# Kernel tuning notes

Measured on AMD Instinct MI355X. Metric: run time of the kernel, lower is better.

Reference implementation:

```python
import jax, jax.numpy as jnp
import numpy as np

N, C, T = 64, 512, 64
P = N * (N - 1) // 2  # 2016 pairs


def _maxpool2x2(h):
    p, c, H, W = h.shape
    return h.reshape(p, c, H // 2, 2, W // 2, 2).max(axis=(3, 5))


def setup_inputs() -> dict:
    key = jax.random.key(0)
    ks = jax.random.split(key, 16)
    s = lambda k, shape, fan: jax.random.normal(k, shape, jnp.float32) * (1.0 / np.sqrt(fan))
    return {
        "x": jax.random.normal(ks[0], (N, C, T), jnp.float32),
        "w_conv1d": s(ks[1], (256, 512), 512),  # Conv1d(512,256,k=1) weight squeezed
        "b_conv1d": jnp.zeros((256,), jnp.float32),
        "w_c1": s(ks[2], (32, 512), 512),       # Conv2d(512,32,1x1)
        "b_c1": jnp.zeros((32,), jnp.float32),
        "w_c2": s(ks[3], (8, 32), 32),          # Conv2d(32,8,1x1)
        "b_c2": jnp.zeros((8,), jnp.float32),
        "w_fc1": s(ks[4], (32, 64), 64),
        "b_fc1": jnp.zeros((32,), jnp.float32),
        "w_fc2": s(ks[5], (8, 32), 32),
        "b_fc2": jnp.zeros((8,), jnp.float32),
        "w_fc3": s(ks[6], (1, 8), 8),
        "b_fc3": jnp.zeros((1,), jnp.float32),
        "w_mlp": s(ks[7], (1, C * T), C * T),   # stand-in my_fc: Linear(512*T,1)
        "b_mlp": jnp.zeros((1,), jnp.float32),
    }


def reference(x, w_conv1d, b_conv1d, w_c1, b_c1, w_c2, b_c2,
              w_fc1, b_fc1, w_fc2, b_fc2, w_fc3, b_fc3, w_mlp, b_mlp):
    # per-sample score head (my_fc stand-in)
    score = jax.nn.sigmoid(x.reshape(N, -1) @ w_mlp.T + b_mlp)  # [N,1]
    # shared conv1d over all samples at once (original does it per-pair)
    f = jnp.einsum("nct,oc->not", x, w_conv1d) + b_conv1d[None, :, None]  # [N,256,T]
    ii, jj = jnp.triu_indices(N, k=1)  # P pairs, same order as the nested loop
    # pairwise correlation matrix: einsum('abd,acd->abc')
    M = jnp.einsum("pct,pdt->pcd", f[ii], f[jj])  # [P,256,256]
    M = M.reshape(P, 512, 32, 4)
    h = jnp.einsum("pchw,oc->pohw", M, w_c1) + b_c1[None, :, None, None]
    h = _maxpool2x2(h)  # [P,32,16,2]
    h = jnp.einsum("pchw,oc->pohw", h, w_c2) + b_c2[None, :, None, None]
    h = _maxpool2x2(h)  # [P,8,8,1]
    v = h.reshape(P, 64)
    v = jax.nn.relu(v @ w_fc1.T + b_fc1)
    v = jax.nn.relu(v @ w_fc2.T + b_fc2)
    group_score = jax.nn.sigmoid(v @ w_fc3.T + b_fc3).reshape(-1)  # [P]
    return score, group_score
```

## Files before the change

### kernel.cpp

```cpp
#include <hip/hip_runtime.h>
#include <hip/hip_bf16.h>
#include <math.h>


typedef __attribute__((ext_vector_type(8))) short short8;
typedef __attribute__((ext_vector_type(4))) float f32x4;

__device__ __forceinline__ unsigned short f2bf(float f) {
    __hip_bfloat16 h = __float2bfloat16(f);
    return *reinterpret_cast<unsigned short*>(&h);
}

__global__ __launch_bounds__(256) void k_prep(
    const float* __restrict__ x, const float* __restrict__ w_conv1d,
    const float* __restrict__ b_conv1d, const float* __restrict__ w_c1,
    const float* __restrict__ w_mlp,
    unsigned short* __restrict__ xxTf, unsigned short* __restrict__ Wbf,
    float* __restrict__ Gb, float* __restrict__ part)
{
    __shared__ float sf[64 * 65];
    int u = blockIdx.x, tid = threadIdx.x;

    if (u < 128) {
        int idx = u * 256 + tid;
        int m = idx >> 7, c4 = (idx & 127) * 4;
        float4 v = *reinterpret_cast<const float4*>(w_conv1d + m * 512 + c4);
        ushort4 uu;
        uu.x = f2bf(v.x); uu.y = f2bf(v.y); uu.z = f2bf(v.z); uu.w = f2bf(v.w);
        int mt = m >> 4, r15 = m & 15;
        int kc = c4 >> 5, k8 = (c4 >> 3) & 3, rem = c4 & 7;
        *reinterpret_cast<ushort4*>(
            Wbf + ((mt * 16 + kc) * 64 + k8 * 16 + r15) * 8 + rem) = uu;
    } else if (u < 256) {
        int b = u - 128;
        int r = b >> 1;
        int cin = (b & 1) * 256 + tid;
        int s = r >> 5, o = r & 31;
        const float* wrow = w_c1 + o * 512 + s;
        const float* wcp  = w_conv1d + cin;
        float pq[4];
        #pragma unroll
        for (int q = 0; q < 4; ++q) {
            float acc = 0.f;
            #pragma unroll 8
            for (int c = q * 64; c < q * 64 + 64; ++c)
                acc += wrow[2 * c] * wcp[c * 512];
            pq[q] = acc;
        }
        float v = ((pq[0] + pq[1]) + pq[2]) + pq[3];
        int m = 256 + r;
        int mt = m >> 4, r15 = m & 15;
        int kc = cin >> 5, k8 = (cin >> 3) & 3, rem = cin & 7;
        Wbf[((mt * 16 + kc) * 64 + k8 * 16 + r15) * 8 + rem] = f2bf(v);
    } else if (u == 256) {
        float* abred = sf;
        Gb[tid] = b_conv1d[tid];
        int r = tid & 63, q = tid >> 6;
        int s = r >> 5, o = r & 31;
        const float* wr2 = w_c1 + o * 512 + s;
        float a = 0.f;
        #pragma unroll 8
        for (int c = q * 64; c < q * 64 + 64; ++c)
            a += wr2[2 * c] * b_conv1d[c];
        abred[tid] = a;
        __syncthreads();
        if (tid < 64)
            Gb[256 + tid] = abred[tid] + abred[tid + 64]
                          + abred[tid + 128] + abred[tid + 192];
    } else if (u < 769) {
        int v = u - 257;
        int n = v >> 3, c0 = (v & 7) * 64;
        float* tile = sf;
        int cl = tid >> 4, t4 = (tid & 15) * 4;
        const float* xp = x + n * 32768 + c0 * 64;
        #pragma unroll
        for (int pp = 0; pp < 4; ++pp) {
            int c = cl + pp * 16;
            float4 vv = *reinterpret_cast<const float4*>(xp + c * 64 + t4);
            tile[(t4 + 0) * 65 + c] = vv.x; tile[(t4 + 1) * 65 + c] = vv.y;
            tile[(t4 + 2) * 65 + c] = vv.z; tile[(t4 + 3) * 65 + c] = vv.w;
        }
        __syncthreads();
        int tl = tid >> 4, cl4 = (tid & 15) * 4;
        int c = c0 + cl4;
        int kc = c >> 5, k8 = (c >> 3) & 3, rem = c & 7;
        #pragma unroll
        for (int pp = 0; pp < 4; ++pp) {
            int t = tl + pp * 16;
            ushort4 uu;
            uu.x = f2bf(tile[t * 65 + cl4 + 0]);
            uu.y = f2bf(tile[t * 65 + cl4 + 1]);
            uu.z = f2bf(tile[t * 65 + cl4 + 2]);
            uu.w = f2bf(tile[t * 65 + cl4 + 3]);
            *reinterpret_cast<ushort4*>(
                xxTf + n * 32768 + ((pp * 16 + kc) * 64 + k8 * 16 + tl) * 8 + rem) = uu;
        }
    } else {
        int v = u - 769;
        int n = v >> 2, c4 = v & 3;
        const float4* x4 = reinterpret_cast<const float4*>(x + n * 32768) + c4 * 2048;
        const float4* w4 = reinterpret_cast<const float4*>(w_mlp) + c4 * 2048;
        float acc = 0.f;
        for (int uu = tid; uu < 2048; uu += 256) {
            float4 a = x4[uu], w = w4[uu];
            acc += a.x * w.x + a.y * w.y + a.z * w.z + a.w * w.w;
        }
        for (int off = 32; off; off >>= 1) acc += __shfl_down(acc, off, 64);
        float* red = sf;
        if ((tid & 63) == 0) red[tid >> 6] = acc;
        __syncthreads();
        if (tid == 0)
            part[n * 4 + c4] = red[0] + red[1] + red[2] + red[3];
    }
}

__global__ __launch_bounds__(256) void k_fgemm(
    const unsigned short* __restrict__ Wbf, const unsigned short* __restrict__ xxTf,
    const float* __restrict__ Gb, unsigned short* __restrict__ FTTb,
    unsigned short* __restrict__ ALb)
{
    int n = blockIdx.x, mg = blockIdx.y, nt = blockIdx.z;
    int tid = threadIdx.x, l = tid & 63, w = tid >> 6;
    int mt = mg * 4 + w;
    int m0 = mt * 16;
    int t0 = nt * 16;
    int r15 = l & 15, kg = l >> 4;
    const unsigned short* ap = Wbf + (size_t)mt * 16 * 512 + l * 8;
    const unsigned short* bp = xxTf + (size_t)n * 32768 + (size_t)nt * 16 * 512 + l * 8;
    f32x4 acc = {0.f, 0.f, 0.f, 0.f};
    #pragma unroll
    for (int ks = 0; ks < 16; ++ks) {
        short8 a = *reinterpret_cast<const short8*>(ap + ks * 512);
        short8 b = *reinterpret_cast<const short8*>(bp + ks * 512);
        acc = __builtin_amdgcn_mfma_f32_16x16x32_bf16(a, b, acc, 0, 0, 0);
    }
    int t = t0 + r15;
    int mrow = m0 + kg * 4;
    float4 gb = *reinterpret_cast<const float4*>(Gb + mrow);
    float gbv[4] = {gb.x, gb.y, gb.z, gb.w};
    if (m0 < 256) {
        #pragma unroll
        for (int r = 0; r < 4; ++r) {
            int m = mrow + r;
            int e = m & 127, s = m >> 7, kp = s * 64 + t;
            int off = (((e << 8) + (kp << 1)) ^ ((e & 7) << 4)) >> 1;
            FTTb[n * 16384 + off] = f2bf(acc[r] + gbv[r]);
        }
    } else {
        #pragma unroll
        for (int r = 0; r < 4; ++r) {
            int m = mrow + r;
            int rr = m - 256, o = rr & 31, sA = rr >> 5, kp = sA * 64 + t;
            int off = (((o << 8) + (kp << 1)) ^ ((o & 7) << 4)) >> 1;
            ALb[n * 4096 + off] = f2bf(acc[r] + gbv[r]);
        }
    }
}

__global__ __launch_bounds__(256) void k_pairs(
    const char* __restrict__ FTTb, const char* __restrict__ ALb,
    const float* __restrict__ b_c1, const float* __restrict__ w_c2,
    const float* __restrict__ b_c2, const float* __restrict__ w_fc1,
    const float* __restrict__ b_fc1, const float* __restrict__ w_fc2,
    const float* __restrict__ b_fc2, const float* __restrict__ w_fc3,
    const float* __restrict__ b_fc3, const float* __restrict__ part,
    const float* __restrict__ bm, float* __restrict__ out)
{
    __shared__ uint4 smq[2560];
    char* sm = (char*)smq;
    int p = blockIdx.x;
    int i = 0, rem = p;
    while (rem >= 63 - i) { rem -= 63 - i; ++i; }
    int j = i + 1 + rem;
    int tid = threadIdx.x;

    if (p == 0 && tid >= 128 && tid < 192) {
        int n = tid - 128;
        float s = part[n * 4] + part[n * 4 + 1] + part[n * 4 + 2]
                + part[n * 4 + 3] + bm[0];
        out[n] = 1.f / (1.f + expf(-s));
    }

    {
        const uint4* sA = reinterpret_cast<const uint4*>(ALb + (size_t)i * 8192);
        uint4* dA = reinterpret_cast<uint4*>(sm);
        #pragma unroll
        for (int u = 0; u < 2; ++u) dA[tid + 256 * u] = sA[tid + 256 * u];
        const uint4* sB = reinterpret_cast<const uint4*>(FTTb + (size_t)j * 32768);
        uint4* dB = reinterpret_cast<uint4*>(sm + 8192);
        #pragma unroll
        for (int u = 0; u < 8; ++u) dB[tid + 256 * u] = sB[tid + 256 * u];
    }
    __syncthreads();

    int l = tid & 63, wid = tid >> 6;
    int col = l & 15;
    int lk16 = (l >> 4) << 4;
    int xr = (col & 7) << 4;
    int oa0 = col, oa1 = col + 16;
    int e0 = wid * 32 + col, e1 = e0 + 16;

    f32x4 acc00 = {0.f,0.f,0.f,0.f}, acc01 = {0.f,0.f,0.f,0.f};
    f32x4 acc10 = {0.f,0.f,0.f,0.f}, acc11 = {0.f,0.f,0.f,0.f};
    #pragma unroll
    for (int ks = 0; ks < 4; ++ks) {
        int kb = ks * 64 + lk16;
        short8 a0 = *reinterpret_cast<const short8*>(sm + (((oa0 << 8) + kb) ^ xr));
        short8 a1 = *reinterpret_cast<const short8*>(sm + (((oa1 << 8) + kb) ^ xr));
        short8 b0 = *reinterpret_cast<const short8*>(sm + 8192 + (((e0 << 8) + kb) ^ xr));
        short8 b1 = *reinterpret_cast<const short8*>(sm + 8192 + (((e1 << 8) + kb) ^ xr));
        acc00 = __builtin_amdgcn_mfma_f32_16x16x32_bf16(a0, b0, acc00, 0, 0, 0);
        acc01 = __builtin_amdgcn_mfma_f32_16x16x32_bf16(a0, b1, acc01, 0, 0, 0);
        acc10 = __builtin_amdgcn_mfma_f32_16x16x32_bf16(a1, b0, acc10, 0, 0, 0);
        acc11 = __builtin_amdgcn_mfma_f32_16x16x32_bf16(a1, b1, acc11, 0, 0, 0);
    }
    __syncthreads();

    float* H = (float*)sm;
    int rowbase = (l >> 4) * 4;
    #pragma unroll
    for (int r4 = 0; r4 < 4; ++r4) {
        int o0 = rowbase + r4, o1 = o0 + 16;
        float bb0 = b_c1[o0], bb1 = b_c1[o1];
        H[o0 * 132 + e0] = acc00[r4] + bb0;
        H[o0 * 132 + e1] = acc01[r4] + bb0;
        H[o1 * 132 + e0] = acc10[r4] + bb1;
        H[o1 * 132 + e1] = acc11[r4] + bb1;
    }
    __syncthreads();

    float* PL = (float*)(sm + 17408);
    for (int idx = tid; idx < 1024; idx += 256) {
        int o = idx >> 5, h2 = (idx >> 1) & 15, w2 = idx & 1;
        const float* hp = H + o * 132 + h2 * 8 + w2 * 2;
        PL[o * 32 + h2 * 2 + w2] =
            fmaxf(fmaxf(hp[0], hp[1]), fmaxf(hp[4], hp[5]));
    }
    __syncthreads();

    float* C2 = (float*)(sm + 21504);
    {
        int o2 = tid >> 5, pos = tid & 31;
        float a2 = b_c2[o2];
        #pragma unroll 8
        for (int o = 0; o < 32; ++o) a2 += w_c2[o2 * 32 + o] * PL[o * 32 + pos];
        C2[o2 * 32 + pos] = a2;
    }
    __syncthreads();

    float* V = (float*)(sm + 22528);
    if (tid < 64) {
        int o2 = tid >> 3, h3 = tid & 7;
        const float* cp = C2 + o2 * 32 + h3 * 4;
        V[tid] = fmaxf(fmaxf(cp[0], cp[1]), fmaxf(cp[2], cp[3]));
    }
    __syncthreads();

    float* R1 = (float*)(sm + 22784);
    if (tid < 32) {
        float a = b_fc1[tid];
        const float* wr = w_fc1 + tid * 64;
        #pragma unroll 8
        for (int u = 0; u < 64; ++u) a += wr[u] * V[u];
        R1[tid] = fmaxf(a, 0.f);
    }
    __syncthreads();

    float* R2 = (float*)(sm + 22912);
    if (tid < 8) {
        float a = b_fc2[tid];
        #pragma unroll 8
        for (int u = 0; u < 32; ++u) a += w_fc2[tid * 32 + u] * R1[u];
        R2[tid] = fmaxf(a, 0.f);
    }
    __syncthreads();

    if (tid == 0) {
        float a = b_fc3[0];
        #pragma unroll
        for (int u = 0; u < 8; ++u) a += w_fc3[u] * R2[u];
        out[64 + p] = 1.f / (1.f + expf(-a));
    }
}

extern "C" void kernel_launch(void* const* d_in, const int* in_sizes, int n_in,
                              void* d_out, int out_size, void* d_ws, size_t ws_size,
                              hipStream_t stream) {
    const float* x        = (const float*)d_in[0];
    const float* w_conv1d = (const float*)d_in[1];
    const float* b_conv1d = (const float*)d_in[2];
    const float* w_c1     = (const float*)d_in[3];
    const float* b_c1     = (const float*)d_in[4];
    const float* w_c2     = (const float*)d_in[5];
    const float* b_c2     = (const float*)d_in[6];
    const float* w_fc1    = (const float*)d_in[7];
    const float* b_fc1    = (const float*)d_in[8];
    const float* w_fc2    = (const float*)d_in[9];
    const float* b_fc2    = (const float*)d_in[10];
    const float* w_fc3    = (const float*)d_in[11];
    const float* b_fc3    = (const float*)d_in[12];
    const float* w_mlp    = (const float*)d_in[13];
    const float* b_mlp    = (const float*)d_in[14];
    float* out = (float*)d_out;

    char* base = (char*)d_ws;
    unsigned short* xxTf = (unsigned short*)(base);
    unsigned short* FTTb = (unsigned short*)(base + 4194304);
    unsigned short* ALb  = (unsigned short*)(base + 6291456);
    unsigned short* Wbf  = (unsigned short*)(base + 6815744);
    float*          Gb   = (float*)(base + 7143424);
    float*          part = (float*)(base + 7145472);

    hipLaunchKernelGGL(k_prep, dim3(1025), dim3(256), 0, stream,
                       x, w_conv1d, b_conv1d, w_c1, w_mlp,
                       xxTf, Wbf, Gb, part);
    hipLaunchKernelGGL(k_fgemm, dim3(64, 5, 4), dim3(256), 0, stream,
                       Wbf, xxTf, Gb, FTTb, ALb);
    hipLaunchKernelGGL(k_pairs, dim3(2016), dim3(256), 0, stream,
                       (const char*)FTTb, (const char*)ALb,
                       b_c1, w_c2, b_c2, w_fc1, b_fc1,
                       w_fc2, b_fc2, w_fc3, b_fc3, part, b_mlp, out);
}
```

Measured before the change: 118.7 us.

## Process one pair per wavefront with MFMA-fragment-ordered global layout and shuffle maxpool

The fgemm epilogue now writes F and the conv1 projection straight into MFMA fragment order, so k_pairs can load operands from global memory with no LDS staging. Each wavefront handles a whole pair: it computes the full 32x128 tile, does the first 2x2 maxpool with lane shuffles, and runs the small MLP tail in its own LDS slice with no block barriers. The grid shrinks from 2016 to 504 blocks. In exchange each wave holds 64 accumulator registers and issues more global loads, which may lower occupancy.

New measurement: 123.3 us. +3.9%, slower.

```diff
diff --git a/kernel.cpp b/kernel.cpp
--- a/kernel.cpp
+++ b/kernel.cpp
@@ -116,8 +116,8 @@
 
 __global__ __launch_bounds__(256) void k_fgemm(
     const unsigned short* __restrict__ Wbf, const unsigned short* __restrict__ xxTf,
-    const float* __restrict__ Gb, unsigned short* __restrict__ FTTb,
-    unsigned short* __restrict__ ALb)
+    const float* __restrict__ Gb, unsigned short* __restrict__ FTf,
+    unsigned short* __restrict__ ALf)
 {
     int n = blockIdx.x, mg = blockIdx.y, nt = blockIdx.z;
     int tid = threadIdx.x, l = tid & 63, w = tid >> 6;
@@ -138,27 +138,32 @@
     int mrow = m0 + kg * 4;
     float4 gb = *reinterpret_cast<const float4*>(Gb + mrow);
     float gbv[4] = {gb.x, gb.y, gb.z, gb.w};
+    int ksl = t >> 5, kgrp = (t >> 3) & 3, uu = t & 7;
     if (m0 < 256) {
         #pragma unroll
         for (int r = 0; r < 4; ++r) {
             int m = mrow + r;
-            int e = m & 127, s = m >> 7, kp = s * 64 + t;
-            int off = (((e << 8) + (kp << 1)) ^ ((e & 7) << 4)) >> 1;
-            FTTb[n * 16384 + off] = f2bf(acc[r] + gbv[r]);
+            int e = m & 127, s = m >> 7;
+            int et = e >> 4, l15 = e & 15;
+            int ks = s * 2 + ksl;
+            FTf[n * 16384 + ((et * 4 + ks) * 64 + kgrp * 16 + l15) * 8 + uu]
+                = f2bf(acc[r] + gbv[r]);
         }
     } else {
         #pragma unroll
         for (int r = 0; r < 4; ++r) {
             int m = mrow + r;
-            int rr = m - 256, o = rr & 31, sA = rr >> 5, kp = sA * 64 + t;
-            int off = (((o << 8) + (kp << 1)) ^ ((o & 7) << 4)) >> 1;
-            ALb[n * 4096 + off] = f2bf(acc[r] + gbv[r]);
+            int rr = m - 256, o = rr & 31, sA = rr >> 5;
+            int oa = o >> 4, l15 = o & 15;
+            int ks = sA * 2 + ksl;
+            ALf[n * 4096 + ((oa * 4 + ks) * 64 + kgrp * 16 + l15) * 8 + uu]
+                = f2bf(acc[r] + gbv[r]);
         }
     }
 }
 
 __global__ __launch_bounds__(256) void k_pairs(
-    const char* __restrict__ FTTb, const char* __restrict__ ALb,
+    const unsigned short* __restrict__ FTf, const unsigned short* __restrict__ ALf,
     const float* __restrict__ b_c1, const float* __restrict__ w_c2,
     const float* __restrict__ b_c2, const float* __restrict__ w_fc1,
     const float* __restrict__ b_fc1, const float* __restrict__ w_fc2,
@@ -166,120 +171,100 @@
     const float* __restrict__ b_fc3, const float* __restrict__ part,
     const float* __restrict__ bm, float* __restrict__ out)
 {
-    __shared__ uint4 smq[2560];
-    char* sm = (char*)smq;
-    int p = blockIdx.x;
-    int i = 0, rem = p;
-    while (rem >= 63 - i) { rem -= 63 - i; ++i; }
-    int j = i + 1 + rem;
-    int tid = threadIdx.x;
-
-    if (p == 0 && tid >= 128 && tid < 192) {
-        int n = tid - 128;
+    __shared__ float sm[4 * 1440];
+    int tid = threadIdx.x, w = tid >> 6, l = tid & 63;
+    int wp = blockIdx.x * 4 + w;
+
+    if (blockIdx.x == 0 && w == 0) {
+        int n = l;
         float s = part[n * 4] + part[n * 4 + 1] + part[n * 4 + 2]
                 + part[n * 4 + 3] + bm[0];
         out[n] = 1.f / (1.f + expf(-s));
     }
 
-    {
-        const uint4* sA = reinterpret_cast<const uint4*>(ALb + (size_t)i * 8192);
-        uint4* dA = reinterpret_cast<uint4*>(sm);
-        #pragma unroll
-        for (int u = 0; u < 2; ++u) dA[tid + 256 * u] = sA[tid + 256 * u];
-        const uint4* sB = reinterpret_cast<const uint4*>(FTTb + (size_t)j * 32768);
-        uint4* dB = reinterpret_cast<uint4*>(sm + 8192);
-        #pragma unroll
-        for (int u = 0; u < 8; ++u) dB[tid + 256 * u] = sB[tid + 256 * u];
-    }
-    __syncthreads();
-
-    int l = tid & 63, wid = tid >> 6;
-    int col = l & 15;
-    int lk16 = (l >> 4) << 4;
-    int xr = (col & 7) << 4;
-    int oa0 = col, oa1 = col + 16;
-    int e0 = wid * 32 + col, e1 = e0 + 16;
-
-    f32x4 acc00 = {0.f,0.f,0.f,0.f}, acc01 = {0.f,0.f,0.f,0.f};
-    f32x4 acc10 = {0.f,0.f,0.f,0.f}, acc11 = {0.f,0.f,0.f,0.f};
+    int i = 0, rem = wp;
+    while (rem >= 63 - i) { rem -= 63 - i; ++i; }
+    int j = i + 1 + rem;
+
+    const unsigned short* ap = ALf + i * 4096;
+    const unsigned short* bp = FTf + (size_t)j * 16384;
+
+    f32x4 acc[2][8] = {};
     #pragma unroll
     for (int ks = 0; ks < 4; ++ks) {
-        int kb = ks * 64 + lk16;
-        short8 a0 = *reinterpret_cast<const short8*>(sm + (((oa0 << 8) + kb) ^ xr));
-        short8 a1 = *reinterpret_cast<const short8*>(sm + (((oa1 << 8) + kb) ^ xr));
-        short8 b0 = *reinterpret_cast<const short8*>(sm + 8192 + (((e0 << 8) + kb) ^ xr));
-        short8 b1 = *reinterpret_cast<const short8*>(sm + 8192 + (((e1 << 8) + kb) ^ xr));
-        acc00 = __builtin_amdgcn_mfma_f32_16x16x32_bf16(a0, b0, acc00, 0, 0, 0);
-        acc01 = __builtin_amdgcn_mfma_f32_16x16x32_bf16(a0, b1, acc01, 0, 0, 0);
-        acc10 = __builtin_amdgcn_mfma_f32_16x16x32_bf16(a1, b0, acc10, 0, 0, 0);
-        acc11 = __builtin_amdgcn_mfma_f32_16x16x32_bf16(a1, b1, acc11, 0, 0, 0);
-    }
-    __syncthreads();
-
-    float* H = (float*)sm;
-    int rowbase = (l >> 4) * 4;
-    #pragma unroll
-    for (int r4 = 0; r4 < 4; ++r4) {
-        int o0 = rowbase + r4, o1 = o0 + 16;
-        float bb0 = b_c1[o0], bb1 = b_c1[o1];
-        H[o0 * 132 + e0] = acc00[r4] + bb0;
-        H[o0 * 132 + e1] = acc01[r4] + bb0;
-        H[o1 * 132 + e0] = acc10[r4] + bb1;
-        H[o1 * 132 + e1] = acc11[r4] + bb1;
-    }
-    __syncthreads();
-
-    float* PL = (float*)(sm + 17408);
-    for (int idx = tid; idx < 1024; idx += 256) {
-        int o = idx >> 5, h2 = (idx >> 1) & 15, w2 = idx & 1;
-        const float* hp = H + o * 132 + h2 * 8 + w2 * 2;
-        PL[o * 32 + h2 * 2 + w2] =
-            fmaxf(fmaxf(hp[0], hp[1]), fmaxf(hp[4], hp[5]));
-    }
-    __syncthreads();
-
-    float* C2 = (float*)(sm + 21504);
-    {
-        int o2 = tid >> 5, pos = tid & 31;
+        short8 a0 = *reinterpret_cast<const short8*>(ap + ((0 + ks) * 64 + l) * 8);
+        short8 a1 = *reinterpret_cast<const short8*>(ap + ((4 + ks) * 64 + l) * 8);
+        #pragma unroll
+        for (int et = 0; et < 8; ++et) {
+            short8 b = *reinterpret_cast<const short8*>(bp + ((et * 4 + ks) * 64 + l) * 8);
+            acc[0][et] = __builtin_amdgcn_mfma_f32_16x16x32_bf16(a0, b, acc[0][et], 0, 0, 0);
+            acc[1][et] = __builtin_amdgcn_mfma_f32_16x16x32_bf16(a1, b, acc[1][et], 0, 0, 0);
+        }
+    }
+
+    float* PL = sm + w * 1440;
+    float* C2 = PL + 1056;
+    float* V  = C2 + 264;
+    float* R1 = V + 64;
+    float* R2 = R1 + 32;
+
+    int c = l & 15, g = l >> 4;
+    bool valid = (c == 0) | (c == 2) | (c == 8) | (c == 10);
+    int phb = ((c >> 3) << 1) + ((c >> 1) & 1);
+    float bc[2][4];
+    #pragma unroll
+    for (int oa = 0; oa < 2; ++oa)
+        #pragma unroll
+        for (int r = 0; r < 4; ++r) bc[oa][r] = b_c1[oa * 16 + g * 4 + r];
+    #pragma unroll
+    for (int oa = 0; oa < 2; ++oa)
+        #pragma unroll
+        for (int et = 0; et < 8; ++et)
+            #pragma unroll
+            for (int r = 0; r < 4; ++r) {
+                float v = acc[oa][et][r];
+                v = fmaxf(v, __shfl_xor(v, 1, 64));
+                v = fmaxf(v, __shfl_xor(v, 4, 64));
+                if (valid) {
+                    int o = oa * 16 + g * 4 + r;
+                    PL[o * 33 + et * 4 + phb] = v + bc[oa][r];
+                }
+            }
+
+    #pragma unroll
+    for (int q = 0; q < 4; ++q) {
+        int idx = q * 64 + l;
+        int o2 = idx >> 5, pos = idx & 31;
         float a2 = b_c2[o2];
         #pragma unroll 8
-        for (int o = 0; o < 32; ++o) a2 += w_c2[o2 * 32 + o] * PL[o * 32 + pos];
-        C2[o2 * 32 + pos] = a2;
-    }
-    __syncthreads();
-
-    float* V = (float*)(sm + 22528);
-    if (tid < 64) {
-        int o2 = tid >> 3, h3 = tid & 7;
-        const float* cp = C2 + o2 * 32 + h3 * 4;
-        V[tid] = fmaxf(fmaxf(cp[0], cp[1]), fmaxf(cp[2], cp[3]));
-    }
-    __syncthreads();
-
-    float* R1 = (float*)(sm + 22784);
-    if (tid < 32) {
-        float a = b_fc1[tid];
-        const float* wr = w_fc1 + tid * 64;
+        for (int o = 0; o < 32; ++o) a2 += w_c2[o2 * 32 + o] * PL[o * 33 + pos];
+        C2[o2 * 33 + pos] = a2;
+    }
+
+    {
+        int o2 = l >> 3, h3 = l & 7;
+        const float* cp = C2 + o2 * 33 + h3 * 4;
+        V[l] = fmaxf(fmaxf(cp[0], cp[1]), fmaxf(cp[2], cp[3]));
+    }
+
+    if (l < 32) {
+        float a = b_fc1[l];
+        const float* wr = w_fc1 + l * 64;
         #pragma unroll 8
         for (int u = 0; u < 64; ++u) a += wr[u] * V[u];
-        R1[tid] = fmaxf(a, 0.f);
-    }
-    __syncthreads();
-
-    float* R2 = (float*)(sm + 22912);
-    if (tid < 8) {
-        float a = b_fc2[tid];
+        R1[l] = fmaxf(a, 0.f);
+    }
+    if (l < 8) {
+        float a = b_fc2[l];
         #pragma unroll 8
-        for (int u = 0; u < 32; ++u) a += w_fc2[tid * 32 + u] * R1[u];
-        R2[tid] = fmaxf(a, 0.f);
-    }
-    __syncthreads();
-
-    if (tid == 0) {
+        for (int u = 0; u < 32; ++u) a += w_fc2[l * 32 + u] * R1[u];
+        R2[l] = fmaxf(a, 0.f);
+    }
+    if (l == 0) {
         float a = b_fc3[0];
         #pragma unroll
         for (int u = 0; u < 8; ++u) a += w_fc3[u] * R2[u];
-        out[64 + p] = 1.f / (1.f + expf(-a));
+        out[64 + wp] = 1.f / (1.f + expf(-a));
     }
 }
 
@@ -305,8 +290,8 @@
 
     char* base = (char*)d_ws;
     unsigned short* xxTf = (unsigned short*)(base);
-    unsigned short* FTTb = (unsigned short*)(base + 4194304);
-    unsigned short* ALb  = (unsigned short*)(base + 6291456);
+    unsigned short* FTf  = (unsigned short*)(base + 4194304);
+    unsigned short* ALf  = (unsigned short*)(base + 6291456);
     unsigned short* Wbf  = (unsigned short*)(base + 6815744);
     float*          Gb   = (float*)(base + 7143424);
     float*          part = (float*)(base + 7145472);
@@ -315,9 +300,8 @@
                        x, w_conv1d, b_conv1d, w_c1, w_mlp,
                        xxTf, Wbf, Gb, part);
     hipLaunchKernelGGL(k_fgemm, dim3(64, 5, 4), dim3(256), 0, stream,
-                       Wbf, xxTf, Gb, FTTb, ALb);
-    hipLaunchKernelGGL(k_pairs, dim3(2016), dim3(256), 0, stream,
-                       (const char*)FTTb, (const char*)ALb,
-                       b_c1, w_c2, b_c2, w_fc1, b_fc1,
+                       Wbf, xxTf, Gb, FTf, ALf);
+    hipLaunchKernelGGL(k_pairs, dim3(504), dim3(256), 0, stream,
+                       FTf, ALf, b_c1, w_c2, b_c2, w_fc1, b_fc1,
                        w_fc2, b_fc2, w_fc3, b_fc3, part, b_mlp, out);
 }
```
